# Optimization experiments

Hardware: AMD Instinct MI355X
Metric: run time of the kernel (lower is better)

## Reference

```python
import jax, jax.numpy as jnp
import numpy as np

N_HEADS = 8
D_EMBED = 1024
D_CROSS = 768
D_HEAD = D_EMBED // N_HEADS


def setup_inputs() -> dict:
    key = jax.random.key(0)
    ks = jax.random.split(key, 10)
    B, SQ, SKV = 8, 4096, 77
    scale_e = 1.0 / np.sqrt(D_EMBED)
    scale_c = 1.0 / np.sqrt(D_CROSS)
    return {
        "x": jax.random.normal(ks[0], (B, SQ, D_EMBED), dtype=jnp.float32),
        "y": jax.random.normal(ks[1], (B, SKV, D_CROSS), dtype=jnp.float32),
        # weights stored as [in, out] so projection is x @ W + b
        "Wq": jax.random.normal(ks[2], (D_EMBED, D_EMBED), dtype=jnp.float32) * scale_e,
        "bq": jnp.zeros((D_EMBED,), dtype=jnp.float32),
        "Wk": jax.random.normal(ks[3], (D_CROSS, D_EMBED), dtype=jnp.float32) * scale_c,
        "bk": jnp.zeros((D_EMBED,), dtype=jnp.float32),
        "Wv": jax.random.normal(ks[4], (D_CROSS, D_EMBED), dtype=jnp.float32) * scale_c,
        "bv": jnp.zeros((D_EMBED,), dtype=jnp.float32),
        "Wo": jax.random.normal(ks[5], (D_EMBED, D_EMBED), dtype=jnp.float32) * scale_e,
        "bo": jnp.zeros((D_EMBED,), dtype=jnp.float32),
    }


def reference(x, y, Wq, bq, Wk, bk, Wv, bv, Wo, bo):
    B, SQ, _ = x.shape
    # projections
    q = x @ Wq + bq                      # [B, SQ, D_EMBED]
    k = y @ Wk + bk                      # [B, SKV, D_EMBED]
    v = y @ Wv + bv                      # [B, SKV, D_EMBED]
    # split heads -> [B, H, S, Dh]
    q = q.reshape(B, SQ, N_HEADS, D_HEAD).transpose(0, 2, 1, 3)
    k = k.reshape(B, -1, N_HEADS, D_HEAD).transpose(0, 2, 1, 3)
    v = v.reshape(B, -1, N_HEADS, D_HEAD).transpose(0, 2, 1, 3)
    # attention: q@k^T / sqrt(d_head), softmax, @v
    scale = 1.0 / jnp.sqrt(jnp.asarray(D_HEAD, dtype=q.dtype))
    weight = jnp.einsum("bhqd,bhkd->bhqk", q, k) * scale  # [B, H, SQ, SKV]
    weight = jax.nn.softmax(weight, axis=-1)
    out = jnp.einsum("bhqk,bhkd->bhqd", weight, v)        # [B, H, SQ, Dh]
    out = out.transpose(0, 2, 1, 3).reshape(B, SQ, D_EMBED)
    return out @ Wo + bo
```

## Files before the change

kernel.cpp:

```cpp
#include <hip/hip_runtime.h>

typedef _Float16 half_t;
typedef _Float16 half8 __attribute__((ext_vector_type(8)));
typedef float f32x4 __attribute__((ext_vector_type(4)));

#define D_EMBED   1024
#define D_CROSS   768
#define N_HEADS   8
#define D_HEAD    128
#define BATCH     8
#define SEQ_Q     4096
#define SEQ_KV    77
#define SKV_PAD   80
#define NKV       (N_HEADS*SKV_PAD)
#define NKV_PAD   768
#define M_Q       (BATCH*SEQ_Q)

#define WS_S     ((size_t)0)
#define WS_WQC   (WS_S    + (size_t)M_Q*NKV*2)
#define WS_WOT   (WS_WQC  + (size_t)D_EMBED*D_EMBED*2)
#define WS_WKVT  (WS_WOT  + (size_t)D_EMBED*D_EMBED*2)
#define WS_YH    (WS_WKVT + (size_t)2*D_EMBED*D_CROSS*2)
#define WS_KV    (WS_YH   + (size_t)BATCH*SKV_PAD*D_CROSS*2)
#define WS_BKV   (WS_KV   + (size_t)BATCH*SKV_PAD*2*D_EMBED*2)
#define WS_BT1   (WS_BKV  + (size_t)2*D_EMBED*4)
#define WS_BT2   (WS_BT1  + (size_t)BATCH*NKV_PAD*D_EMBED*2)
#define WS_C1    (WS_BT2  + (size_t)BATCH*D_EMBED*NKV*2)

#define ATTN_SCALE 0.08838834764831845f

__device__ __forceinline__ void gload_lds16(const void* g, void* lds) {
  __builtin_amdgcn_global_load_lds(
      (const __attribute__((address_space(1))) unsigned int*)g,
      (__attribute__((address_space(3))) unsigned int*)lds, 16, 0, 0);
}
__device__ __forceinline__ void BAR() {
  __builtin_amdgcn_s_barrier();
  __builtin_amdgcn_sched_barrier(0);
}

__global__ void cast_f32_f16(const float* __restrict__ src, half_t* __restrict__ dst) {
  int i = blockIdx.x * 256 + threadIdx.x;
  f32x4 a = *(const f32x4*)(src + (size_t)i*8);
  f32x4 b = *(const f32x4*)(src + (size_t)i*8 + 4);
  half8 h;
#pragma unroll
  for (int j = 0; j < 4; ++j) { h[j] = (half_t)a[j]; h[j+4] = (half_t)b[j]; }
  *(half8*)(dst + (size_t)i*8) = h;
}

__global__ void transpose_f32f16(const float* __restrict__ src, half_t* __restrict__ dst,
                                 int K, int N) {
  __shared__ float tile[32][33];
  int n0 = blockIdx.x * 32, k0 = blockIdx.y * 32;
  int tx = threadIdx.x, ty = threadIdx.y;
#pragma unroll
  for (int j = 0; j < 4; ++j)
    tile[ty + j*8][tx] = src[(size_t)(k0 + ty + j*8)*N + n0 + tx];
  __syncthreads();
#pragma unroll
  for (int j = 0; j < 4; ++j)
    dst[(size_t)(n0 + ty + j*8)*K + k0 + tx] = (half_t)tile[tx][ty + j*8];
}

__global__ void convert_pad_y(const float* __restrict__ y, half_t* __restrict__ yh) {
  int idx = blockIdx.x * 256 + threadIdx.x;
  int r = idx / D_CROSS, col = idx - r*D_CROSS;
  int b = r / SKV_PAD, s = r - b*SKV_PAD;
  yh[idx] = (s < SEQ_KV) ? (half_t)y[(size_t)(b*SEQ_KV + s)*D_CROSS + col] : (half_t)0.f;
}

__global__ void concat_bias(const float* __restrict__ bk, const float* __restrict__ bv,
                            float* __restrict__ bkv) {
  int i = blockIdx.x * 256 + threadIdx.x;
  bkv[i] = (i < D_EMBED) ? bk[i] : bv[i - D_EMBED];
}

__global__ __launch_bounds__(256, 3)
void gemm_kv(const half_t* __restrict__ A, const half_t* __restrict__ Bt,
             const float* __restrict__ bias, half_t* __restrict__ C,
             int M, int N, int K) {
  __shared__ half_t As[3][128*32];
  __shared__ half_t Bs[2][128*32];
  const int tid = threadIdx.x;
  const int l = tid & 63, w = tid >> 6;
  const int l4 = l & 15, lh = l >> 4;
  const int bn0 = blockIdx.x * 128, bm0 = blockIdx.y * 128;
  const int wr = w >> 1, wc = w & 1;
  const int rslot = lh << 4;
  f32x4 acc[4][4] = {};
  const int nk = K >> 5;
  const int srow = w*16 + (l >> 2);
  const int scol = (l & 3)*8;

  auto stageB = [&](int kt, int bb) {
    const half_t* g = Bt + (size_t)(bn0 + srow)*K + scol + kt*32;
    gload_lds16(g,                 (char*)Bs[bb] + w*1024);
    gload_lds16(g + (size_t)64*K,  (char*)Bs[bb] + 4096 + w*1024);
  };
  auto stageA = [&](int kt, int bb) {
    const half_t* g = A + (size_t)(bm0 + srow)*K + scol + kt*32;
    gload_lds16(g,                 (char*)As[bb] + w*1024);
    gload_lds16(g + (size_t)64*K,  (char*)As[bb] + 4096 + w*1024);
  };
  auto compute = [&](int ab, int bb) {
    half8 af[4], bf[4];
#pragma unroll
    for (int m = 0; m < 4; ++m)
      af[m] = *(const half8*)((const char*)As[ab] + (size_t)(wr*64 + m*16 + l4)*64 + rslot);
#pragma unroll
    for (int n = 0; n < 4; ++n)
      bf[n] = *(const half8*)((const char*)Bs[bb] + (size_t)(wc*64 + n*16 + l4)*64 + rslot);
#pragma unroll
    for (int m = 0; m < 4; ++m)
#pragma unroll
      for (int n = 0; n < 4; ++n)
        acc[m][n] = __builtin_amdgcn_mfma_f32_16x16x32_f16(af[m], bf[n], acc[m][n], 0, 0, 0);
  };

  stageA(0, 0); stageA(1, 1); stageB(0, 0);
  asm volatile("s_waitcnt vmcnt(0)" ::: "memory");
  BAR();
  int aCur = 0, aP2 = 2;
  for (int t = 0; t < nk; ++t) {
    if (t + 1 < nk) stageB(t + 1, (t + 1) & 1);
    if (t + 2 < nk) stageA(t + 2, aP2);
    compute(aCur, t & 1);
    if (t + 1 < nk) {
      if (t + 2 < nk) { asm volatile("s_waitcnt vmcnt(2)" ::: "memory"); }
      else            { asm volatile("s_waitcnt vmcnt(0)" ::: "memory"); }
      BAR();
    }
    aCur = (aCur == 2) ? 0 : aCur + 1;
    aP2  = (aP2  == 2) ? 0 : aP2  + 1;
  }

  const int cb = bn0 + wc*64, rb = bm0 + wr*64;
#pragma unroll
  for (int n = 0; n < 4; ++n) {
    const int col = cb + n*16 + l4;
    const float bvv = bias[col];
#pragma unroll
    for (int m = 0; m < 4; ++m)
#pragma unroll
      for (int j = 0; j < 4; ++j)
        C[(size_t)(rb + m*16 + lh*4 + j)*N + col] = (half_t)(acc[m][n][j] + bvv);
  }
}

__global__ __launch_bounds__(256, 2)
void w1_build(const half_t* __restrict__ kvb, const half_t* __restrict__ Wqc,
              half_t* __restrict__ Bt1) {
  __shared__ half_t K_lds[80*136];
  const int blk = blockIdx.x;
  const int b = blk >> 3, h = blk & 7;
  const int tid = threadIdx.x;
  const int l = tid & 63, w = tid >> 6;
  const int l4 = l & 15, lh = l >> 4;
  for (int i = tid; i < 80*16; i += 256) {
    int s = i >> 4, d = (i & 15) << 3;
    *(half8*)(K_lds + s*136 + d) =
        *(const half8*)(kvb + (size_t)(b*SKV_PAD + s)*2048 + h*128 + d);
  }
  __syncthreads();
  for (int c = 0; c < 4; ++c) {
    f32x4 acc[5][4] = {};
#pragma unroll
    for (int kt = 0; kt < 4; ++kt) {
      half8 af[5], bf[4];
#pragma unroll
      for (int m = 0; m < 5; ++m)
        af[m] = *(const half8*)(K_lds + (size_t)(m*16 + l4)*136 + kt*32 + lh*8);
#pragma unroll
      for (int n = 0; n < 4; ++n)
        bf[n] = *(const half8*)(Wqc + (size_t)(w*256 + c*64 + n*16 + l4)*1024 + h*128 + kt*32 + lh*8);
#pragma unroll
      for (int m = 0; m < 5; ++m)
#pragma unroll
        for (int n = 0; n < 4; ++n)
          acc[m][n] = __builtin_amdgcn_mfma_f32_16x16x32_f16(af[m], bf[n], acc[m][n], 0, 0, 0);
    }
#pragma unroll
    for (int n = 0; n < 4; ++n) {
      const int colk = w*256 + c*64 + n*16 + l4;
#pragma unroll
      for (int m = 0; m < 5; ++m)
#pragma unroll
        for (int j = 0; j < 4; ++j) {
          const int r = h*SKV_PAD + m*16 + lh*4 + j;
          size_t byte = ((size_t)(b*NKV_PAD + r))*2048 + (size_t)(colk >> 6)*128
                        + ((size_t)(((colk >> 3) & 7) ^ (r & 7)) << 4) + ((colk & 7) << 1);
          *(half_t*)((char*)Bt1 + byte) = (half_t)(acc[m][n][j]*ATTN_SCALE);
        }
    }
  }
}

__global__ __launch_bounds__(256, 2)
void w2_build(const half_t* __restrict__ kvb, const half_t* __restrict__ Wot,
              half_t* __restrict__ Bt2) {
  __shared__ half_t V_lds[80*136];
  const int blk = blockIdx.x;
  const int b = blk >> 3, h = blk & 7;
  const int tid = threadIdx.x;
  const int l = tid & 63, w = tid >> 6;
  const int l4 = l & 15, lh = l >> 4;
  for (int i = tid; i < 80*16; i += 256) {
    int s = i >> 4, d = (i & 15) << 3;
    *(half8*)(V_lds + s*136 + d) =
        *(const half8*)(kvb + (size_t)(b*SKV_PAD + s)*2048 + 1024 + h*128 + d);
  }
  __syncthreads();
  for (int c = 0; c < 4; ++c) {
    f32x4 acc[4][5] = {};
#pragma unroll
    for (int kt = 0; kt < 4; ++kt) {
      half8 af[4], bf[5];
#pragma unroll
      for (int m = 0; m < 4; ++m)
        af[m] = *(const half8*)(Wot + (size_t)(w*256 + c*64 + m*16 + l4)*1024 + h*128 + kt*32 + lh*8);
#pragma unroll
      for (int n = 0; n < 5; ++n)
        bf[n] = *(const half8*)(V_lds + (size_t)(n*16 + l4)*136 + kt*32 + lh*8);
#pragma unroll
      for (int m = 0; m < 4; ++m)
#pragma unroll
        for (int n = 0; n < 5; ++n)
          acc[m][n] = __builtin_amdgcn_mfma_f32_16x16x32_f16(af[m], bf[n], acc[m][n], 0, 0, 0);
    }
#pragma unroll
    for (int m = 0; m < 4; ++m) {
#pragma unroll
      for (int j = 0; j < 4; ++j) {
        const int nrow = w*256 + c*64 + m*16 + lh*4 + j;
        const size_t rowbase = ((size_t)(b*1024 + nrow))*1280;
#pragma unroll
        for (int n = 0; n < 5; ++n) {
          const int cc = h*80 + n*16 + l4;
          size_t byte = rowbase + (size_t)(cc >> 6)*128
                        + ((size_t)(((cc >> 3) & 7) ^ (nrow & 7)) << 4) + ((cc & 7) << 1);
          *(half_t*)((char*)Bt2 + byte) = (half_t)acc[m][n][j];
        }
      }
    }
  }
}

__global__ void c1_build(const half_t* __restrict__ kvb, const float* __restrict__ bq,
                         float* __restrict__ c1) {
  int idx = blockIdx.x * 256 + threadIdx.x;
  int b = idx / NKV, n = idx - b*NKV;
  int h = n / SKV_PAD, s = n - h*SKV_PAD;
  const half_t* kp = kvb + (size_t)(b*SKV_PAD + s)*2048 + h*128;
  float acc = 0.f;
#pragma unroll 8
  for (int d = 0; d < 128; ++d) acc += bq[h*128 + d] * (float)kp[d];
  c1[idx] = acc * ATTN_SCALE;
}

__global__ __launch_bounds__(512, 2)
void fused_sv(const float* __restrict__ X, const half_t* __restrict__ Bt1,
              const float* __restrict__ c1, const half_t* __restrict__ Bt2,
              const float* __restrict__ bo, float* __restrict__ out) {
  __shared__ half_t S_lds[64*640];
  __shared__ half_t x_lds[2][64*64];
  const int tid = threadIdx.x;
  const int l = tid & 63, w = tid >> 6;
  const int l4 = l & 15, lh = l >> 4;
  const int k7 = l4 & 7;

  const int lin = ((int)blockIdx.x & 7)*64 + ((int)blockIdx.x >> 3);
  const int batch = lin >> 6;
  const int row0 = batch*SEQ_Q + (lin & 63)*64;
  const half_t* W1 = Bt1 + (size_t)batch*NKV_PAD*1024;
  const half_t* W2 = Bt2 + (size_t)batch*1024*NKV;
  const float* c1b = c1 + batch*NKV;

  f32x4 sacc[4][5] = {};
  const int nfb = w*5;

  const int xrow = tid >> 3, xc8 = tid & 7;
  const float* xg = X + (size_t)(row0 + xrow)*1024 + xc8*8;
  f32x4 xa, xb;
  auto xload = [&](int kc) {
    const float* g = xg + kc*64;
    xa = *(const f32x4*)g; xb = *(const f32x4*)(g + 4);
  };
  auto xwrite = [&](int buf) {
    half8 h;
#pragma unroll
    for (int e = 0; e < 4; ++e) { h[e] = (half_t)xa[e]; h[e+4] = (half_t)xb[e]; }
    *(half8*)((char*)x_lds[buf] + xrow*128 + ((xc8 ^ (xrow & 7)) << 4)) = h;
  };

  xload(0); xwrite(0);
  __syncthreads();

  for (int kc = 0; kc < 16; ++kc) {
    if (kc + 1 < 16) xload(kc + 1);
    const char* xc = (const char*)x_lds[kc & 1];
#pragma unroll
    for (int kk = 0; kk < 2; ++kk) {
      half8 af[4];
#pragma unroll
      for (int m = 0; m < 4; ++m)
        af[m] = *(const half8*)(xc + (size_t)(m*16 + l4)*128 + (((kk*4 + lh) ^ k7) << 4));
#pragma unroll
      for (int nf = 0; nf < 5; ++nf) {
        const int nrow = (nfb + nf)*16 + l4;
        half8 bfv = *(const half8*)((const char*)W1 + (size_t)nrow*2048 + (size_t)kc*128
                                    + (((kk*4 + lh) ^ k7) << 4));
#pragma unroll
        for (int m = 0; m < 4; ++m)
          sacc[m][nf] = __builtin_amdgcn_mfma_f32_16x16x32_f16(af[m], bfv, sacc[m][nf], 0, 0, 0);
      }
    }
    if (kc + 1 < 16) {
      xwrite((kc + 1) & 1);
      __syncthreads();
    }
  }

#pragma unroll
  for (int nf = 0; nf < 5; ++nf) {
    const int col = (nfb + nf)*16 + l4;
#pragma unroll
    for (int m = 0; m < 4; ++m)
#pragma unroll
      for (int j = 0; j < 4; ++j) {
        const int row = m*16 + lh*4 + j;
        size_t byte = (size_t)row*1280 + (size_t)(col >> 6)*128
                      + ((size_t)(((col >> 3) & 7) ^ (row & 7)) << 4) + ((col & 7) << 1);
        *(half_t*)((char*)S_lds + byte) = (half_t)sacc[m][nf][j];
      }
  }
  __syncthreads();

  {
    const int row = tid >> 3, h = tid & 7;
    const int key = row & 7;
    char* base = (char*)S_lds + (size_t)row*1280;
    float fv[10][8];
    float mx = -1e30f;
#pragma unroll
    for (int i = 0; i < 10; ++i) {
      const int ls = h*10 + i;
      half8 v = *(const half8*)(base + (size_t)(ls >> 3)*128 + ((size_t)((ls & 7) ^ key) << 4));
      f32x4 ca = *(const f32x4*)(c1b + h*80 + i*8);
      f32x4 cb = *(const f32x4*)(c1b + h*80 + i*8 + 4);
#pragma unroll
      for (int j = 0; j < 8; ++j) {
        const float cc = (j < 4) ? ca[j] : cb[j - 4];
        const float sv = (float)v[j] + cc;
        const bool ok = (i*8 + j) < SEQ_KV;
        fv[i][j] = ok ? sv : -1e30f;
        if (ok) mx = fmaxf(mx, sv);
      }
    }
    float sm = 0.f;
#pragma unroll
    for (int i = 0; i < 10; ++i)
#pragma unroll
      for (int j = 0; j < 8; ++j) { float e = __expf(fv[i][j] - mx); sm += e; fv[i][j] = e; }
    const float inv = 1.f / sm;
#pragma unroll
    for (int i = 0; i < 10; ++i) {
      const int ls = h*10 + i;
      half8 t;
#pragma unroll
      for (int j = 0; j < 8; ++j) t[j] = (half_t)(fv[i][j] * inv);
      *(half8*)(base + (size_t)(ls >> 3)*128 + ((size_t)((ls & 7) ^ key) << 4)) = t;
    }
  }
  __syncthreads();

  f32x4 oacc[4][8] = {};
  const int ncb = w*128;
  for (int ks = 0; ks < 20; ++ks) {
    const size_t koff = (size_t)(ks >> 1)*128 + ((((ks & 1)*4 + lh) ^ k7) << 4);
    half8 af[4];
#pragma unroll
    for (int m = 0; m < 4; ++m)
      af[m] = *(const half8*)((const char*)S_lds + (size_t)(m*16 + l4)*1280 + koff);
#pragma unroll
    for (int nf = 0; nf < 8; ++nf) {
      const int nrow = ncb + nf*16 + l4;
      half8 bfv = *(const half8*)((const char*)W2 + (size_t)nrow*1280 + koff);
#pragma unroll
      for (int m = 0; m < 4; ++m)
        oacc[m][nf] = __builtin_amdgcn_mfma_f32_16x16x32_f16(af[m], bfv, oacc[m][nf], 0, 0, 0);
    }
  }

#pragma unroll
  for (int nf = 0; nf < 8; ++nf) {
    const int col = ncb + nf*16 + l4;
    const float bvv = bo[col];
#pragma unroll
    for (int m = 0; m < 4; ++m)
#pragma unroll
      for (int j = 0; j < 4; ++j) {
        const int row = row0 + m*16 + lh*4 + j;
        out[(size_t)row*1024 + col] = oacc[m][nf][j] + bvv;
      }
  }
}

extern "C" void kernel_launch(void* const* d_in, const int* in_sizes, int n_in,
                              void* d_out, int out_size, void* d_ws, size_t ws_size,
                              hipStream_t stream) {
  (void)in_sizes; (void)n_in; (void)out_size; (void)ws_size;
  const float* x  = (const float*)d_in[0];
  const float* y  = (const float*)d_in[1];
  const float* Wq = (const float*)d_in[2];
  const float* bq = (const float*)d_in[3];
  const float* Wk = (const float*)d_in[4];
  const float* bk = (const float*)d_in[5];
  const float* Wv = (const float*)d_in[6];
  const float* bv = (const float*)d_in[7];
  const float* Wo = (const float*)d_in[8];
  const float* bo = (const float*)d_in[9];

  char* ws = (char*)d_ws;
  half_t* Wqc  = (half_t*)(ws + WS_WQC);
  half_t* Wot  = (half_t*)(ws + WS_WOT);
  half_t* Wkvt = (half_t*)(ws + WS_WKVT);
  half_t* yh   = (half_t*)(ws + WS_YH);
  half_t* kvb  = (half_t*)(ws + WS_KV);
  float*  bkv  = (float*)(ws + WS_BKV);
  half_t* Bt1  = (half_t*)(ws + WS_BT1);
  half_t* Bt2  = (half_t*)(ws + WS_BT2);
  float*  c1   = (float*)(ws + WS_C1);

  dim3 tb(32, 8);
  cast_f32_f16<<<512, 256, 0, stream>>>(Wq, Wqc);
  transpose_f32f16<<<dim3(32, 32), tb, 0, stream>>>(Wo, Wot, 1024, 1024);
  transpose_f32f16<<<dim3(32, 24), tb, 0, stream>>>(Wk, Wkvt, 768, 1024);
  transpose_f32f16<<<dim3(32, 24), tb, 0, stream>>>(Wv, Wkvt + (size_t)1024*768, 768, 1024);
  convert_pad_y<<<BATCH*SKV_PAD*D_CROSS/256, 256, 0, stream>>>(y, yh);
  concat_bias<<<2*D_EMBED/256, 256, 0, stream>>>(bk, bv, bkv);

  gemm_kv<<<dim3(16, 5), 256, 0, stream>>>(yh, Wkvt, bkv, kvb, BATCH*SKV_PAD, 2048, 768);

  c1_build<<<BATCH*NKV/256, 256, 0, stream>>>(kvb, bq, c1);
  w1_build<<<BATCH*N_HEADS, 256, 0, stream>>>(kvb, Wqc, Bt1);
  w2_build<<<BATCH*N_HEADS, 256, 0, stream>>>(kvb, Wot, Bt2);

  fused_sv<<<512, 512, 0, stream>>>(x, Bt1, c1, Bt2, bo, (float*)d_out);
}
```

Before: 259.3 us.

## Double-buffer weight fragment loads and split output GEMM into two passes in fused_sv

Weight B-fragments for both GEMMs in fused_sv are now prefetched one k-step ahead into register double buffers, so global loads overlap the MFMA work. MFMA bursts are wrapped in s_setprio. The output GEMM is split into two 64-column passes to cut accumulator registers. __syncthreads is replaced by an explicit lgkmcnt wait plus a BAR macro, and launch bounds drop to one block per SIMD set, which trades occupancy for more registers.

New measurement: 248.1 us. -4.3%, faster.

```diff
diff --git a/kernel.cpp b/kernel.cpp
--- a/kernel.cpp
+++ b/kernel.cpp
@@ -258,7 +258,7 @@
   c1[idx] = acc * ATTN_SCALE;
 }
 
-__global__ __launch_bounds__(512, 2)
+__global__ __launch_bounds__(512, 1)
 void fused_sv(const float* __restrict__ X, const half_t* __restrict__ Bt1,
               const float* __restrict__ c1, const half_t* __restrict__ Bt2,
               const float* __restrict__ bo, float* __restrict__ out) {
@@ -272,8 +272,8 @@
   const int lin = ((int)blockIdx.x & 7)*64 + ((int)blockIdx.x >> 3);
   const int batch = lin >> 6;
   const int row0 = batch*SEQ_Q + (lin & 63)*64;
-  const half_t* W1 = Bt1 + (size_t)batch*NKV_PAD*1024;
-  const half_t* W2 = Bt2 + (size_t)batch*1024*NKV;
+  const char* W1 = (const char*)(Bt1 + (size_t)batch*NKV_PAD*1024);
+  const char* W2 = (const char*)(Bt2 + (size_t)batch*1024*NKV);
   const float* c1b = c1 + batch*NKV;
 
   f32x4 sacc[4][5] = {};
@@ -293,31 +293,44 @@
     *(half8*)((char*)x_lds[buf] + xrow*128 + ((xc8 ^ (xrow & 7)) << 4)) = h;
   };
 
+  half8 b0[5], b1[5];
+  auto bload = [&](int t, half8* dst) {
+    const int kc = t >> 1, kk = t & 1;
+    const size_t koff = (size_t)kc*128 + (size_t)(((kk*4 + lh) ^ k7) << 4);
+#pragma unroll
+    for (int nf = 0; nf < 5; ++nf)
+      dst[nf] = *(const half8*)(W1 + (size_t)((nfb + nf)*16 + l4)*2048 + koff);
+  };
+  auto smfma = [&](const half8* bf, int kc, int kk) {
+    const char* xc = (const char*)x_lds[kc & 1];
+    half8 af[4];
+#pragma unroll
+    for (int m = 0; m < 4; ++m)
+      af[m] = *(const half8*)(xc + (size_t)(m*16 + l4)*128 + (((kk*4 + lh) ^ k7) << 4));
+    __builtin_amdgcn_s_setprio(1);
+#pragma unroll
+    for (int nf = 0; nf < 5; ++nf)
+#pragma unroll
+      for (int m = 0; m < 4; ++m)
+        sacc[m][nf] = __builtin_amdgcn_mfma_f32_16x16x32_f16(af[m], bf[nf], sacc[m][nf], 0, 0, 0);
+    __builtin_amdgcn_s_setprio(0);
+  };
+
   xload(0); xwrite(0);
-  __syncthreads();
+  bload(0, b0);
+  asm volatile("s_waitcnt lgkmcnt(0)" ::: "memory");
+  BAR();
 
   for (int kc = 0; kc < 16; ++kc) {
     if (kc + 1 < 16) xload(kc + 1);
-    const char* xc = (const char*)x_lds[kc & 1];
-#pragma unroll
-    for (int kk = 0; kk < 2; ++kk) {
-      half8 af[4];
-#pragma unroll
-      for (int m = 0; m < 4; ++m)
-        af[m] = *(const half8*)(xc + (size_t)(m*16 + l4)*128 + (((kk*4 + lh) ^ k7) << 4));
-#pragma unroll
-      for (int nf = 0; nf < 5; ++nf) {
-        const int nrow = (nfb + nf)*16 + l4;
-        half8 bfv = *(const half8*)((const char*)W1 + (size_t)nrow*2048 + (size_t)kc*128
-                                    + (((kk*4 + lh) ^ k7) << 4));
-#pragma unroll
-        for (int m = 0; m < 4; ++m)
-          sacc[m][nf] = __builtin_amdgcn_mfma_f32_16x16x32_f16(af[m], bfv, sacc[m][nf], 0, 0, 0);
-      }
-    }
+    bload(2*kc + 1, b1);
+    smfma(b0, kc, 0);
+    if (2*kc + 2 < 32) bload(2*kc + 2, b0);
+    smfma(b1, kc, 1);
     if (kc + 1 < 16) {
       xwrite((kc + 1) & 1);
-      __syncthreads();
+      asm volatile("s_waitcnt lgkmcnt(0)" ::: "memory");
+      BAR();
     }
   }
 
@@ -334,7 +347,8 @@
         *(half_t*)((char*)S_lds + byte) = (half_t)sacc[m][nf][j];
       }
   }
-  __syncthreads();
+  asm volatile("s_waitcnt lgkmcnt(0)" ::: "memory");
+  BAR();
 
   {
     const int row = tid >> 3, h = tid & 7;
@@ -372,37 +386,55 @@
       *(half8*)(base + (size_t)(ls >> 3)*128 + ((size_t)((ls & 7) ^ key) << 4)) = t;
     }
   }
-  __syncthreads();
-
-  f32x4 oacc[4][8] = {};
-  const int ncb = w*128;
-  for (int ks = 0; ks < 20; ++ks) {
-    const size_t koff = (size_t)(ks >> 1)*128 + ((((ks & 1)*4 + lh) ^ k7) << 4);
-    half8 af[4];
-#pragma unroll
-    for (int m = 0; m < 4; ++m)
-      af[m] = *(const half8*)((const char*)S_lds + (size_t)(m*16 + l4)*1280 + koff);
-#pragma unroll
-    for (int nf = 0; nf < 8; ++nf) {
-      const int nrow = ncb + nf*16 + l4;
-      half8 bfv = *(const half8*)((const char*)W2 + (size_t)nrow*1280 + koff);
+  asm volatile("s_waitcnt lgkmcnt(0)" ::: "memory");
+  BAR();
+
+#pragma unroll 1
+  for (int pass = 0; pass < 2; ++pass) {
+    f32x4 oacc[4][4] = {};
+    half8 p0[4], p1[4];
+    const int ncb = w*128 + pass*64;
+    auto pbload = [&](int ks, half8* dst) {
+      const size_t koff = (size_t)(ks >> 1)*128 + (size_t)((((ks & 1)*4 + lh) ^ k7) << 4);
+#pragma unroll
+      for (int nf = 0; nf < 4; ++nf)
+        dst[nf] = *(const half8*)(W2 + (size_t)(ncb + nf*16 + l4)*1280 + koff);
+    };
+    auto pmfma = [&](const half8* bf, int ks) {
+      const size_t koff = (size_t)(ks >> 1)*128 + (size_t)((((ks & 1)*4 + lh) ^ k7) << 4);
+      half8 af[4];
 #pragma unroll
       for (int m = 0; m < 4; ++m)
-        oacc[m][nf] = __builtin_amdgcn_mfma_f32_16x16x32_f16(af[m], bfv, oacc[m][nf], 0, 0, 0);
-    }
-  }
-
-#pragma unroll
-  for (int nf = 0; nf < 8; ++nf) {
-    const int col = ncb + nf*16 + l4;
-    const float bvv = bo[col];
-#pragma unroll
-    for (int m = 0; m < 4; ++m)
-#pragma unroll
-      for (int j = 0; j < 4; ++j) {
-        const int row = row0 + m*16 + lh*4 + j;
-        out[(size_t)row*1024 + col] = oacc[m][nf][j] + bvv;
-      }
+        af[m] = *(const half8*)((const char*)S_lds + (size_t)(m*16 + l4)*1280 + koff);
+      __builtin_amdgcn_s_setprio(1);
+#pragma unroll
+      for (int nf = 0; nf < 4; ++nf)
+#pragma unroll
+        for (int m = 0; m < 4; ++m)
+          oacc[m][nf] = __builtin_amdgcn_mfma_f32_16x16x32_f16(af[m], bf[nf], oacc[m][nf], 0, 0, 0);
+      __builtin_amdgcn_s_setprio(0);
+    };
+
+    pbload(0, p0);
+    for (int ks = 0; ks < 20; ks += 2) {
+      pbload(ks + 1, p1);
+      pmfma(p0, ks);
+      if (ks + 2 < 20) pbload(ks + 2, p0);
+      pmfma(p1, ks + 1);
+    }
+
+#pragma unroll
+    for (int nf = 0; nf < 4; ++nf) {
+      const int col = ncb + nf*16 + l4;
+      const float bvv = bo[col];
+#pragma unroll
+      for (int m = 0; m < 4; ++m)
+#pragma unroll
+        for (int j = 0; j < 4; ++j) {
+          const int row = row0 + m*16 + lh*4 + j;
+          out[(size_t)row*1024 + col] = oacc[m][nf][j] + bvv;
+        }
+    }
   }
 }
 
```

## Stage Bt1/Bt2 weight tiles through LDS with register-prefetched double buffering

Applied to the files above, without the earlier changes.

The fused score/output kernel used to read the per-batch folded weight matrices (Bt1, Bt2) directly from global memory inside its MFMA loops. It now copies them cooperatively into LDS, double-buffered and prefetched through registers, into a single 144KB shared buffer that is reused for the score tile. The weight builders now write plain row-major layouts instead of pre-swizzled ones. Occupancy drops to one block per CU, and MFMA sections are wrapped in s_setprio, which adds more barriers per iteration and increases LDS pressure.

After: 247.7 us. -4.5%, faster.

```diff
diff --git a/kernel.cpp b/kernel.cpp
--- a/kernel.cpp
+++ b/kernel.cpp
@@ -188,9 +188,7 @@
 #pragma unroll
         for (int j = 0; j < 4; ++j) {
           const int r = h*SKV_PAD + m*16 + lh*4 + j;
-          size_t byte = ((size_t)(b*NKV_PAD + r))*2048 + (size_t)(colk >> 6)*128
-                        + ((size_t)(((colk >> 3) & 7) ^ (r & 7)) << 4) + ((colk & 7) << 1);
-          *(half_t*)((char*)Bt1 + byte) = (half_t)(acc[m][n][j]*ATTN_SCALE);
+          Bt1[((size_t)(b*NKV_PAD + r))*1024 + colk] = (half_t)(acc[m][n][j]*ATTN_SCALE);
         }
     }
   }
@@ -233,13 +231,10 @@
 #pragma unroll
       for (int j = 0; j < 4; ++j) {
         const int nrow = w*256 + c*64 + m*16 + lh*4 + j;
-        const size_t rowbase = ((size_t)(b*1024 + nrow))*1280;
 #pragma unroll
         for (int n = 0; n < 5; ++n) {
           const int cc = h*80 + n*16 + l4;
-          size_t byte = rowbase + (size_t)(cc >> 6)*128
-                        + ((size_t)(((cc >> 3) & 7) ^ (nrow & 7)) << 4) + ((cc & 7) << 1);
-          *(half_t*)((char*)Bt2 + byte) = (half_t)acc[m][n][j];
+          Bt2[((size_t)(b*1024 + nrow))*640 + cc] = (half_t)acc[m][n][j];
         }
       }
     }
@@ -258,12 +253,18 @@
   c1[idx] = acc * ATTN_SCALE;
 }
 
-__global__ __launch_bounds__(512, 2)
+__global__ __launch_bounds__(512, 1)
 void fused_sv(const float* __restrict__ X, const half_t* __restrict__ Bt1,
               const float* __restrict__ c1, const half_t* __restrict__ Bt2,
               const float* __restrict__ bo, float* __restrict__ out) {
-  __shared__ half_t S_lds[64*640];
-  __shared__ half_t x_lds[2][64*64];
+  __shared__ char LDS[147456];
+  char* const Bb0 = LDS;
+  char* const Bb1 = LDS + 51200;
+  char* const Xb0 = LDS + 102400;
+  char* const Xb1 = LDS + 110592;
+  char* const SL  = LDS;
+  char* const WB  = LDS + 81920;
+
   const int tid = threadIdx.x;
   const int l = tid & 63, w = tid >> 6;
   const int l4 = l & 15, lh = l >> 4;
@@ -282,44 +283,91 @@
   const int xrow = tid >> 3, xc8 = tid & 7;
   const float* xg = X + (size_t)(row0 + xrow)*1024 + xc8*8;
   f32x4 xa, xb;
-  auto xload = [&](int kc) {
-    const float* g = xg + kc*64;
+  auto xload = [&](int xc) {
+    const float* g = xg + xc*64;
     xa = *(const f32x4*)g; xb = *(const f32x4*)(g + 4);
   };
-  auto xwrite = [&](int buf) {
+  const int xslot = ((xc8 ^ (xrow & 7)) << 4);
+  auto xwrite = [&](char* buf) {
     half8 h;
 #pragma unroll
     for (int e = 0; e < 4; ++e) { h[e] = (half_t)xa[e]; h[e+4] = (half_t)xb[e]; }
-    *(half8*)((char*)x_lds[buf] + xrow*128 + ((xc8 ^ (xrow & 7)) << 4)) = h;
-  };
-
-  xload(0); xwrite(0);
-  __syncthreads();
-
-  for (int kc = 0; kc < 16; ++kc) {
-    if (kc + 1 < 16) xload(kc + 1);
-    const char* xc = (const char*)x_lds[kc & 1];
-#pragma unroll
-    for (int kk = 0; kk < 2; ++kk) {
-      half8 af[4];
+    *(half8*)(buf + xrow*128 + xslot) = h;
+  };
+
+  half8 Br[5];
+  const int brow0s = tid >> 2;
+  const int bslot = tid & 3;
+  auto bload = [&](int kc) {
+    const half_t* g = W1 + (size_t)brow0s*1024 + kc*32 + bslot*8;
+#pragma unroll
+    for (int i = 0; i < 5; ++i)
+      Br[i] = *(const half8*)(g + (size_t)i*128*1024);
+  };
+  auto bwrite = [&](char* buf) {
+#pragma unroll
+    for (int i = 0; i < 5; ++i)
+      *(half8*)(buf + (size_t)(i*128 + brow0s)*80 + bslot*16) = Br[i];
+  };
+
+  auto smfma = [&](const char* bbuf, const char* xbuf, int kk) {
+    half8 bf[5], af[4];
+#pragma unroll
+    for (int nf = 0; nf < 5; ++nf)
+      bf[nf] = *(const half8*)(bbuf + (size_t)((nfb + nf)*16 + l4)*80 + lh*16);
+#pragma unroll
+    for (int m = 0; m < 4; ++m)
+      af[m] = *(const half8*)(xbuf + (size_t)(m*16 + l4)*128 + (((kk*4 + lh) ^ k7) << 4));
+    __builtin_amdgcn_s_setprio(1);
+#pragma unroll
+    for (int nf = 0; nf < 5; ++nf)
 #pragma unroll
       for (int m = 0; m < 4; ++m)
-        af[m] = *(const half8*)(xc + (size_t)(m*16 + l4)*128 + (((kk*4 + lh) ^ k7) << 4));
-#pragma unroll
-      for (int nf = 0; nf < 5; ++nf) {
-        const int nrow = (nfb + nf)*16 + l4;
-        half8 bfv = *(const half8*)((const char*)W1 + (size_t)nrow*2048 + (size_t)kc*128
-                                    + (((kk*4 + lh) ^ k7) << 4));
-#pragma unroll
-        for (int m = 0; m < 4; ++m)
-          sacc[m][nf] = __builtin_amdgcn_mfma_f32_16x16x32_f16(af[m], bfv, sacc[m][nf], 0, 0, 0);
-      }
-    }
-    if (kc + 1 < 16) {
-      xwrite((kc + 1) & 1);
-      __syncthreads();
-    }
-  }
+        sacc[m][nf] = __builtin_amdgcn_mfma_f32_16x16x32_f16(af[m], bf[nf], sacc[m][nf], 0, 0, 0);
+    __builtin_amdgcn_s_setprio(0);
+  };
+
+  bload(0); bwrite(Bb0); bload(1);
+  xload(0); xwrite(Xb0); xload(1);
+  asm volatile("s_waitcnt lgkmcnt(0)" ::: "memory");
+  BAR();
+
+  for (int kc = 0; kc < 32; ++kc) {
+    char* const bcur = (kc & 1) ? Bb1 : Bb0;
+    char* const bnxt = (kc & 1) ? Bb0 : Bb1;
+    char* const xcur = ((kc >> 1) & 1) ? Xb1 : Xb0;
+    if (kc + 1 < 32) {
+      bwrite(bnxt);
+      if (kc + 2 < 32) bload(kc + 2);
+    }
+    if ((kc & 1) == 1 && kc + 1 < 32) {
+      char* const xnxt = (((kc + 1) >> 1) & 1) ? Xb1 : Xb0;
+      xwrite(xnxt);
+      if (kc + 3 < 32) xload((kc + 3) >> 1);
+    }
+    smfma(bcur, xcur, kc & 1);
+    asm volatile("s_waitcnt lgkmcnt(0)" ::: "memory");
+    BAR();
+  }
+
+  half8 Wr[8];
+  const int wrow0s = tid >> 2;
+  const int wslotP = tid & 3;
+  auto wload = [&](int ks) {
+    const half_t* g = W2 + (size_t)wrow0s*640 + ks*32 + wslotP*8;
+#pragma unroll
+    for (int i = 0; i < 8; ++i)
+      Wr[i] = *(const half8*)(g + (size_t)i*128*640);
+  };
+  auto wwrite = [&]() {
+#pragma unroll
+    for (int i = 0; i < 8; ++i) {
+      const int n = i*128 + wrow0s;
+      *(half8*)(WB + (size_t)n*64 + ((wslotP ^ (n & 3)) << 4)) = Wr[i];
+    }
+  };
+
+  wload(0);
 
 #pragma unroll
   for (int nf = 0; nf < 5; ++nf) {
@@ -331,15 +379,19 @@
         const int row = m*16 + lh*4 + j;
         size_t byte = (size_t)row*1280 + (size_t)(col >> 6)*128
                       + ((size_t)(((col >> 3) & 7) ^ (row & 7)) << 4) + ((col & 7) << 1);
-        *(half_t*)((char*)S_lds + byte) = (half_t)sacc[m][nf][j];
+        *(half_t*)(SL + byte) = (half_t)sacc[m][nf][j];
       }
   }
-  __syncthreads();
+  asm volatile("s_waitcnt lgkmcnt(0)" ::: "memory");
+  BAR();
+
+  wwrite();
+  wload(1);
 
   {
     const int row = tid >> 3, h = tid & 7;
     const int key = row & 7;
-    char* base = (char*)S_lds + (size_t)row*1280;
+    char* base = SL + (size_t)row*1280;
     float fv[10][8];
     float mx = -1e30f;
 #pragma unroll
@@ -372,37 +424,53 @@
       *(half8*)(base + (size_t)(ls >> 3)*128 + ((size_t)((ls & 7) ^ key) << 4)) = t;
     }
   }
-  __syncthreads();
-
-  f32x4 oacc[4][8] = {};
-  const int ncb = w*128;
-  for (int ks = 0; ks < 20; ++ks) {
-    const size_t koff = (size_t)(ks >> 1)*128 + ((((ks & 1)*4 + lh) ^ k7) << 4);
-    half8 af[4];
-#pragma unroll
-    for (int m = 0; m < 4; ++m)
-      af[m] = *(const half8*)((const char*)S_lds + (size_t)(m*16 + l4)*1280 + koff);
+  asm volatile("s_waitcnt lgkmcnt(0)" ::: "memory");
+  BAR();
+
+  {
+    f32x4 oacc[4][8] = {};
+    const int ncb = w*128;
+
+    for (int ks = 0; ks < 20; ++ks) {
+      const size_t koff = (size_t)(ks >> 1)*128 + (size_t)((((ks & 1)*4 + lh) ^ k7) << 4);
+      half8 af[4], bf[8];
+#pragma unroll
+      for (int m = 0; m < 4; ++m)
+        af[m] = *(const half8*)(SL + (size_t)(m*16 + l4)*1280 + koff);
+#pragma unroll
+      for (int nf = 0; nf < 8; ++nf) {
+        const int r = ncb + nf*16 + l4;
+        bf[nf] = *(const half8*)(WB + (size_t)r*64 + ((lh ^ (r & 3)) << 4));
+      }
+      __builtin_amdgcn_s_setprio(1);
+#pragma unroll
+      for (int nf = 0; nf < 8; ++nf)
+#pragma unroll
+        for (int m = 0; m < 4; ++m)
+          oacc[m][nf] = __builtin_amdgcn_mfma_f32_16x16x32_f16(af[m], bf[nf], oacc[m][nf], 0, 0, 0);
+      __builtin_amdgcn_s_setprio(0);
+
+      if (ks + 1 < 20) {
+        BAR();
+        wwrite();
+        if (ks + 2 < 20) wload(ks + 2);
+        asm volatile("s_waitcnt lgkmcnt(0)" ::: "memory");
+        BAR();
+      }
+    }
+
 #pragma unroll
     for (int nf = 0; nf < 8; ++nf) {
-      const int nrow = ncb + nf*16 + l4;
-      half8 bfv = *(const half8*)((const char*)W2 + (size_t)nrow*1280 + koff);
+      const int col = ncb + nf*16 + l4;
+      const float bvv = bo[col];
 #pragma unroll
       for (int m = 0; m < 4; ++m)
-        oacc[m][nf] = __builtin_amdgcn_mfma_f32_16x16x32_f16(af[m], bfv, oacc[m][nf], 0, 0, 0);
-    }
-  }
-
-#pragma unroll
-  for (int nf = 0; nf < 8; ++nf) {
-    const int col = ncb + nf*16 + l4;
-    const float bvv = bo[col];
-#pragma unroll
-    for (int m = 0; m < 4; ++m)
-#pragma unroll
-      for (int j = 0; j < 4; ++j) {
-        const int row = row0 + m*16 + lh*4 + j;
-        out[(size_t)row*1024 + col] = oacc[m][nf][j] + bvv;
-      }
+#pragma unroll
+        for (int j = 0; j < 4; ++j) {
+          const int row = row0 + m*16 + lh*4 + j;
+          out[(size_t)row*1024 + col] = oacc[m][nf][j] + bvv;
+        }
+    }
   }
 }
 
```
